# Performance work log

Hardware: AMD Instinct MI355X
Metric: run time of the kernel (lower is better)

The kernel has to match this reference:

```python
import jax, jax.numpy as jnp
import numpy as np

NQ = 4       # num_qubits
DEPTH = 2
NC = 4       # num_classes
DIM = 2 ** NQ
EPS = 1e-5   # BatchNorm1d eps


def _cz_diag():
    # diagonal of the CZ chain on wires (0,1),(1,2),(2,3); wire w -> bit (NQ-1-w)
    d = np.ones(DIM, np.float32)
    for i in range(NQ - 1):
        for k in range(DIM):
            if ((k >> (NQ - 1 - i)) & 1) and ((k >> (NQ - 2 - i)) & 1):
                d[k] *= -1.0
    return jnp.asarray(d.astype(np.complex64))


def _zmat():
    # ZMAT[k, w] = <k|Z_w|k>
    z = np.empty((DIM, NQ), np.float32)
    for k in range(DIM):
        for w in range(NQ):
            z[k, w] = 1.0 - 2.0 * ((k >> (NQ - 1 - w)) & 1)
    return jnp.asarray(z)


CZ_DIAG = _cz_diag()
ZMAT = _zmat()


def _apply_1q(state, gate, wire):
    # state: [B, DIM] complex64; gate: [2,2] (shared) or [B,2,2] (batched)
    B = state.shape[0]
    left, right = 2 ** wire, 2 ** (NQ - 1 - wire)
    s = state.reshape(B, left, 2, right)
    if gate.ndim == 2:
        s = jnp.einsum('ij,bljr->blir', gate, s)
    else:
        s = jnp.einsum('bij,bljr->blir', gate, s)
    return s.reshape(B, DIM)


def _circuit(pooled, weights):
    # pooled: [B, NQ] angles; weights: [DEPTH*NQ]
    B = pooled.shape[0]
    state = jnp.zeros((B, DIM), jnp.complex64).at[:, 0].set(1.0)
    # RX(pooled[:, i]) on wire i  (batched gates)
    for i in range(NQ):
        th = pooled[:, i] * 0.5
        c, s = jnp.cos(th), jnp.sin(th)
        g = jnp.stack([jnp.stack([c, -1j * s], -1),
                       jnp.stack([-1j * s, c], -1)], -2)  # [B,2,2] complex64
        state = _apply_1q(state, g, i)
    idx = 0
    for _ in range(DEPTH):
        # RY(weights[idx]) on each wire (real 2x2, shared across batch)
        for i in range(NQ):
            th = weights[idx] * 0.5
            idx += 1
            c, s = jnp.cos(th), jnp.sin(th)
            g = jnp.stack([jnp.stack([c, -s]), jnp.stack([s, c])])  # [2,2]
            state = _apply_1q(state, g, i)
        # CZ chain = diagonal sign flips
        state = state * CZ_DIAG
    probs = state.real ** 2 + state.imag ** 2          # [B, DIM]
    return probs @ ZMAT                                # [B, NQ] expvals of Z_w


def setup_inputs() -> dict:
    B = 262144
    keys = jax.random.split(jax.random.key(0), 4)
    x = jax.random.normal(keys[0], (B, 1, 12, 12), jnp.float32)
    weights = jax.random.normal(keys[1], (DEPTH * NQ,), jnp.float32)
    W = jax.random.normal(keys[2], (NC, NQ), jnp.float32) * 0.5
    b = jax.random.normal(keys[3], (NC,), jnp.float32) * 0.1
    gamma = jnp.ones((NC,), jnp.float32)
    beta = jnp.zeros((NC,), jnp.float32)
    return {'x': x, 'weights': weights, 'W': W, 'b': b,
            'gamma': gamma, 'beta': beta}


def reference(x, weights, W, b, gamma, beta):
    B = x.shape[0]
    # avg_pool2d(x, 6): [B,1,12,12] -> [B,1,2,2] -> [B,4]
    pooled = x.reshape(B, 1, 2, 6, 2, 6).mean(axis=(3, 5)).reshape(B, NQ)
    q = _circuit(pooled, weights)                      # [B, NQ]
    logits = q @ W.T + b                               # [B, NC]
    # BatchNorm1d, training mode: batch mean / biased variance
    mean = logits.mean(axis=0)
    var = logits.var(axis=0)
    return (logits - mean) / jnp.sqrt(var + EPS) * gamma + beta
```

## Files before the change

kernel.cpp:

```cpp
#include <hip/hip_runtime.h>
#include <hip/hip_bf16.h>


#define PAD 145

__device__ __forceinline__ float bfbits2f(unsigned short u) {
    return __uint_as_float(((unsigned int)u) << 16);
}
__device__ __forceinline__ float ldp(const void* p, int i, bool isbf16) {
    if (isbf16) return bfbits2f(((const unsigned short*)p)[i]);
    return ((const float*)p)[i];
}
__device__ __forceinline__ float fsin(float th) {
    return __builtin_amdgcn_sinf(th * 0.15915494309189535f);
}
__device__ __forceinline__ float fcos(float th) {
    return __builtin_amdgcn_cosf(th * 0.15915494309189535f);
}

__global__ __launch_bounds__(256) void qcircuit_kernel(
    const void* __restrict__ x,
    const void* __restrict__ wts,
    const void* __restrict__ Wm,
    const void* __restrict__ bias,
    const void* __restrict__ gamma,
    float* __restrict__ logits,
    float* __restrict__ partials,
    int B)
{
    const int t = threadIdx.x;
    const bool isbf16 = (*(const unsigned int*)gamma) == 0x3F803F80u;

    __shared__ float lds_elem[64 * PAD];
    __shared__ float lds_pool[256 * 5];
    __shared__ float red[4][8];

    const int s_b = t >> 2, q_b = t & 3;
    const int r0 = (q_b >> 1) * 6, c0 = (q_b & 1) * 6;

#pragma unroll
    for (int T = 0; T < 4; ++T) {
        const size_t sample0 = (size_t)blockIdx.x * 256 + T * 64;

        if (isbf16) {
            const uint2* src = reinterpret_cast<const uint2*>(x) + sample0 * 36;
#pragma unroll
            for (int k = 0; k < 9; ++k) {
                const int f  = t + 256 * k;
                uint2 v = src[f];
                const int e4 = f * 4;
                const int s  = e4 / 144;
                const int e  = e4 - s * 144;
                float* dst = &lds_elem[s * PAD + e];
                dst[0] = __uint_as_float(v.x << 16);
                dst[1] = __uint_as_float(v.x & 0xffff0000u);
                dst[2] = __uint_as_float(v.y << 16);
                dst[3] = __uint_as_float(v.y & 0xffff0000u);
            }
        } else {
            const float4* src = reinterpret_cast<const float4*>(x) + sample0 * 36;
#pragma unroll
            for (int k = 0; k < 9; ++k) {
                const int f  = t + 256 * k;
                float4 v = src[f];
                const int e4 = f * 4;
                const int s  = e4 / 144;
                const int e  = e4 - s * 144;
                float* dst = &lds_elem[s * PAD + e];
                dst[0] = v.x; dst[1] = v.y; dst[2] = v.z; dst[3] = v.w;
            }
        }
        __syncthreads();

        {
            float acc = 0.f;
            const float* base = &lds_elem[s_b * PAD + r0 * 12 + c0];
#pragma unroll
            for (int r = 0; r < 6; ++r)
#pragma unroll
                for (int c = 0; c < 6; ++c) acc += base[r * 12 + c];
            lds_pool[(T * 64 + s_b) * 5 + q_b] = acc;
        }
        __syncthreads();
    }

    const float pscale = 0.5f / 36.0f;
    float cg[4], sg[4];
#pragma unroll
    for (int w = 0; w < 4; ++w) {
        float th = lds_pool[t * 5 + w] * pscale;
        sg[w] = fsin(th);
        cg[w] = fcos(th);
    }

    float f[16];
#pragma unroll
    for (int k = 0; k < 16; ++k) {
        float a0 = (k & 8) ? sg[0] : cg[0];
        float a1 = (k & 4) ? sg[1] : cg[1];
        float a2 = (k & 2) ? sg[2] : cg[2];
        float a3 = (k & 1) ? sg[3] : cg[3];
        f[k] = (a0 * a1) * (a2 * a3);
    }
    float re[16], im[16];
#pragma unroll
    for (int k = 0; k < 16; ++k) {
        int pc = __popc(k) & 3;
        re[k] = (pc == 0) ? f[k] : ((pc == 2) ? -f[k] : 0.f);
        im[k] = (pc == 3) ? f[k] : ((pc == 1) ? -f[k] : 0.f);
    }

    float wc[8], wsn[8];
#pragma unroll
    for (int i = 0; i < 8; ++i) {
        float th = ldp(wts, i, isbf16) * 0.5f;
        wsn[i] = fsin(th);
        wc[i]  = fcos(th);
    }

#pragma unroll
    for (int d = 0; d < 2; ++d) {
#pragma unroll
        for (int w = 0; w < 4; ++w) {
            const float cc = wc[d * 4 + w], ss = wsn[d * 4 + w];
            const int m = 1 << (3 - w);
#pragma unroll
            for (int k0 = 0; k0 < 16; ++k0) {
                if (k0 & m) continue;
                const int k1 = k0 | m;
                float rr0 = re[k0], rr1 = re[k1];
                re[k0] = cc * rr0 - ss * rr1;
                re[k1] = ss * rr0 + cc * rr1;
                float i0 = im[k0], i1 = im[k1];
                im[k0] = cc * i0 - ss * i1;
                im[k1] = ss * i0 + cc * i1;
            }
        }
#pragma unroll
        for (int k = 0; k < 16; ++k) {
            if ((0xB848u >> k) & 1u) { re[k] = -re[k]; im[k] = -im[k]; }
        }
    }

    float pr[16];
#pragma unroll
    for (int k = 0; k < 16; ++k) pr[k] = re[k] * re[k] + im[k] * im[k];
    float q[4];
#pragma unroll
    for (int w = 0; w < 4; ++w) {
        const int m = 1 << (3 - w);
        float acc = 0.f;
#pragma unroll
        for (int k = 0; k < 16; ++k) acc += (k & m) ? -pr[k] : pr[k];
        q[w] = acc;
    }

    float lg[4];
#pragma unroll
    for (int c = 0; c < 4; ++c) {
        float acc = ldp(bias, c, isbf16);
#pragma unroll
        for (int w = 0; w < 4; ++w) acc += q[w] * ldp(Wm, c * 4 + w, isbf16);
        lg[c] = acc;
    }
    const size_t b = (size_t)blockIdx.x * 256 + t;
    reinterpret_cast<float4*>(logits)[b] = make_float4(lg[0], lg[1], lg[2], lg[3]);

    float rs[8];
#pragma unroll
    for (int c = 0; c < 4; ++c) { rs[c] = lg[c]; rs[4 + c] = lg[c] * lg[c]; }
#pragma unroll
    for (int off = 32; off > 0; off >>= 1) {
#pragma unroll
        for (int i = 0; i < 8; ++i) rs[i] += __shfl_down(rs[i], off, 64);
    }
    if ((t & 63) == 0) {
#pragma unroll
        for (int i = 0; i < 8; ++i) red[t >> 6][i] = rs[i];
    }
    __syncthreads();
    if (t < 8) {
        partials[(size_t)blockIdx.x * 8 + t] =
            red[0][t] + red[1][t] + red[2][t] + red[3][t];
    }
}

__global__ __launch_bounds__(256) void reduce_kernel(
    const float* __restrict__ partials, float* __restrict__ finals, int nblocks)
{
    float acc[8] = {0.f, 0.f, 0.f, 0.f, 0.f, 0.f, 0.f, 0.f};
    for (int r = threadIdx.x; r < nblocks; r += 256) {
#pragma unroll
        for (int i = 0; i < 8; ++i) acc[i] += partials[(size_t)r * 8 + i];
    }
#pragma unroll
    for (int off = 32; off > 0; off >>= 1) {
#pragma unroll
        for (int i = 0; i < 8; ++i) acc[i] += __shfl_down(acc[i], off, 64);
    }
    __shared__ float red[4][8];
    if ((threadIdx.x & 63) == 0) {
#pragma unroll
        for (int i = 0; i < 8; ++i) red[threadIdx.x >> 6][i] = acc[i];
    }
    __syncthreads();
    if (threadIdx.x < 8) {
        finals[threadIdx.x] = red[0][threadIdx.x] + red[1][threadIdx.x] +
                              red[2][threadIdx.x] + red[3][threadIdx.x];
    }
}

__global__ __launch_bounds__(256) void bn_kernel(
    const float* __restrict__ logits,
    const float* __restrict__ finals,
    const void* __restrict__ gamma,
    const void* __restrict__ beta,
    void* __restrict__ out,
    int B)
{
    const int b = blockIdx.x * blockDim.x + threadIdx.x;
    if (b >= B) return;
    const bool isbf16 = (*(const unsigned int*)gamma) == 0x3F803F80u;
    const float invB = 1.0f / (float)B;
    float4 l = reinterpret_cast<const float4*>(logits)[b];
    float lv[4] = {l.x, l.y, l.z, l.w};
    float ov[4];
#pragma unroll
    for (int c = 0; c < 4; ++c) {
        float mean = finals[c] * invB;
        float var  = finals[4 + c] * invB - mean * mean;
        float sc   = ldp(gamma, c, isbf16) * rsqrtf(var + 1e-5f);
        ov[c] = (lv[c] - mean) * sc + ldp(beta, c, isbf16);
    }
    if (isbf16) {
        unsigned short ub[4];
#pragma unroll
        for (int c = 0; c < 4; ++c) {
            __hip_bfloat16 h = __float2bfloat16(ov[c]);
            ub[c] = *reinterpret_cast<unsigned short*>(&h);
        }
        reinterpret_cast<ushort4*>(out)[b] = make_ushort4(ub[0], ub[1], ub[2], ub[3]);
    } else {
        reinterpret_cast<float4*>(out)[b] = make_float4(ov[0], ov[1], ov[2], ov[3]);
    }
}

extern "C" void kernel_launch(void* const* d_in, const int* in_sizes, int n_in,
                              void* d_out, int out_size, void* d_ws, size_t ws_size,
                              hipStream_t stream)
{
    const void* x     = d_in[0];
    const void* wts   = d_in[1];
    const void* Wm    = d_in[2];
    const void* bias  = d_in[3];
    const void* gamma = d_in[4];
    const void* beta  = d_in[5];

    const int B = in_sizes[0] / 144;
    const int nblocks = B / 256;

    float* partials = (float*)d_ws;
    float* finals   = (float*)((char*)d_ws + 64 * 1024);
    float* logits   = (float*)((char*)d_ws + 128 * 1024);

    dim3 blk(256);
    qcircuit_kernel<<<dim3(nblocks), blk, 0, stream>>>(x, wts, Wm, bias, gamma,
                                                       logits, partials, B);
    reduce_kernel<<<dim3(1), blk, 0, stream>>>(partials, finals, nblocks);
    bn_kernel<<<dim3((B + 255) / 256), blk, 0, stream>>>(logits, finals, gamma, beta,
                                                         d_out, B);
}
```

Measured before the change: 231.1 us.

## Pre-reduce each image row in registers before staging to LDS

Each thread now loads a whole 12-element image row, reduces it in registers to left and right half sums, and writes only two values per row to a transposed, padded LDS array. This replaces the four-iteration full-tile LDS staging and per-quadrant re-read with one sync and a small column sum per sample. The aim is less LDS traffic and fewer barriers. Each thread now reads a 48-byte row, so global loads are strided per thread rather than perfectly coalesced float4 streams.

```diff
diff --git a/kernel.cpp b/kernel.cpp
--- a/kernel.cpp
+++ b/kernel.cpp
@@ -1,8 +1,6 @@
 #include <hip/hip_runtime.h>
 #include <hip/hip_bf16.h>
 
-
-#define PAD 145
 
 __device__ __forceinline__ float bfbits2f(unsigned short u) {
     return __uint_as_float(((unsigned int)u) << 16);
@@ -31,64 +29,68 @@
     const int t = threadIdx.x;
     const bool isbf16 = (*(const unsigned int*)gamma) == 0x3F803F80u;
 
-    __shared__ float lds_elem[64 * PAD];
-    __shared__ float lds_pool[256 * 5];
+    __shared__ float lds_rows[24 * 257];
     __shared__ float red[4][8];
 
-    const int s_b = t >> 2, q_b = t & 3;
-    const int r0 = (q_b >> 1) * 6, c0 = (q_b & 1) * 6;
-
-#pragma unroll
-    for (int T = 0; T < 4; ++T) {
-        const size_t sample0 = (size_t)blockIdx.x * 256 + T * 64;
-
-        if (isbf16) {
-            const uint2* src = reinterpret_cast<const uint2*>(x) + sample0 * 36;
-#pragma unroll
-            for (int k = 0; k < 9; ++k) {
-                const int f  = t + 256 * k;
-                uint2 v = src[f];
-                const int e4 = f * 4;
-                const int s  = e4 / 144;
-                const int e  = e4 - s * 144;
-                float* dst = &lds_elem[s * PAD + e];
-                dst[0] = __uint_as_float(v.x << 16);
-                dst[1] = __uint_as_float(v.x & 0xffff0000u);
-                dst[2] = __uint_as_float(v.y << 16);
-                dst[3] = __uint_as_float(v.y & 0xffff0000u);
-            }
-        } else {
-            const float4* src = reinterpret_cast<const float4*>(x) + sample0 * 36;
-#pragma unroll
-            for (int k = 0; k < 9; ++k) {
-                const int f  = t + 256 * k;
-                float4 v = src[f];
-                const int e4 = f * 4;
-                const int s  = e4 / 144;
-                const int e  = e4 - s * 144;
-                float* dst = &lds_elem[s * PAD + e];
-                dst[0] = v.x; dst[1] = v.y; dst[2] = v.z; dst[3] = v.w;
-            }
-        }
-        __syncthreads();
-
-        {
-            float acc = 0.f;
-            const float* base = &lds_elem[s_b * PAD + r0 * 12 + c0];
-#pragma unroll
-            for (int r = 0; r < 6; ++r)
-#pragma unroll
-                for (int c = 0; c < 6; ++c) acc += base[r * 12 + c];
-            lds_pool[(T * 64 + s_b) * 5 + q_b] = acc;
-        }
-        __syncthreads();
+    const size_t row0 = (size_t)blockIdx.x * 3072;
+
+    if (isbf16) {
+        const unsigned short* xp = (const unsigned short*)x;
+#pragma unroll
+        for (int j = 0; j < 12; ++j) {
+            const int rl = t + 256 * j;
+            const uint2* p = reinterpret_cast<const uint2*>(xp + (row0 + rl) * 12);
+            uint2 u0 = p[0], u1 = p[1], u2 = p[2];
+            float e0  = __uint_as_float(u0.x << 16);
+            float e1  = __uint_as_float(u0.x & 0xffff0000u);
+            float e2  = __uint_as_float(u0.y << 16);
+            float e3  = __uint_as_float(u0.y & 0xffff0000u);
+            float e4  = __uint_as_float(u1.x << 16);
+            float e5  = __uint_as_float(u1.x & 0xffff0000u);
+            float e6  = __uint_as_float(u1.y << 16);
+            float e7  = __uint_as_float(u1.y & 0xffff0000u);
+            float e8  = __uint_as_float(u2.x << 16);
+            float e9  = __uint_as_float(u2.x & 0xffff0000u);
+            float e10 = __uint_as_float(u2.y << 16);
+            float e11 = __uint_as_float(u2.y & 0xffff0000u);
+            float L = ((e0 + e1) + (e2 + e3)) + (e4 + e5);
+            float R = ((e6 + e7) + (e8 + e9)) + (e10 + e11);
+            const int s = rl / 12;
+            const int r = rl - 12 * s;
+            lds_rows[(2 * r + 0) * 257 + s] = L;
+            lds_rows[(2 * r + 1) * 257 + s] = R;
+        }
+    } else {
+        const float* xp = (const float*)x;
+#pragma unroll
+        for (int j = 0; j < 12; ++j) {
+            const int rl = t + 256 * j;
+            const float4* p = reinterpret_cast<const float4*>(xp + (row0 + rl) * 12);
+            float4 a = p[0], b4 = p[1], c4 = p[2];
+            float L = ((a.x + a.y) + (a.z + a.w)) + (b4.x + b4.y);
+            float R = ((b4.z + b4.w) + (c4.x + c4.y)) + (c4.z + c4.w);
+            const int s = rl / 12;
+            const int r = rl - 12 * s;
+            lds_rows[(2 * r + 0) * 257 + s] = L;
+            lds_rows[(2 * r + 1) * 257 + s] = R;
+        }
+    }
+    __syncthreads();
+
+    float quad[4] = {0.f, 0.f, 0.f, 0.f};
+#pragma unroll
+    for (int r = 0; r < 12; ++r) {
+        float L = lds_rows[(2 * r + 0) * 257 + t];
+        float R = lds_rows[(2 * r + 1) * 257 + t];
+        if (r < 6) { quad[0] += L; quad[1] += R; }
+        else       { quad[2] += L; quad[3] += R; }
     }
 
     const float pscale = 0.5f / 36.0f;
     float cg[4], sg[4];
 #pragma unroll
     for (int w = 0; w < 4; ++w) {
-        float th = lds_pool[t * 5 + w] * pscale;
+        float th = quad[w] * pscale;
         sg[w] = fsin(th);
         cg[w] = fcos(th);
     }
```

New measurement: 233.1 us. Within noise of the previous version (+0.9%).
